# Kernel optimization log

Measured on AMD Instinct MI355X. Metric: run time of the kernel, lower is better.

The kernel has to match this reference:

```python
import jax, jax.numpy as jnp
import numpy as np

HIDDEN = 1024
NUM_HEADS = 16
HEAD_DIM = 64
B, S = 2, 2048


def setup_inputs() -> dict:
    key = jax.random.key(0)
    k1, k2, k3 = jax.random.split(key, 3)
    x = jax.random.normal(k1, (B, S, HIDDEN), dtype=jnp.float32)
    # xavier-uniform style scaling for the projection weights
    lim_qkv = (6.0 / (HIDDEN + 3 * NUM_HEADS * HEAD_DIM)) ** 0.5
    lim_o = (6.0 / (NUM_HEADS * HEAD_DIM + HIDDEN)) ** 0.5
    w_qkv = jax.random.uniform(k2, (HIDDEN, 3 * NUM_HEADS * HEAD_DIM), jnp.float32, -lim_qkv, lim_qkv)
    w_o = jax.random.uniform(k3, (NUM_HEADS * HEAD_DIM, HIDDEN), jnp.float32, -lim_o, lim_o)
    return {"x": x, "w_qkv": w_qkv, "w_o": w_o}


def reference(x, w_qkv, w_o):
    b, s, _ = x.shape
    qkv = jnp.einsum('bsh,hf->bsf', x, w_qkv)               # [b, s, 3*H*D]
    qkv = qkv.reshape(b, s, 3, NUM_HEADS, HEAD_DIM)
    q = jnp.transpose(qkv[:, :, 0], (0, 2, 1, 3))           # [b, h, s, d]
    k = jnp.transpose(qkv[:, :, 1], (0, 2, 3, 1))           # [b, h, d, s]
    v = jnp.transpose(qkv[:, :, 2], (0, 2, 1, 3))           # [b, h, s, d]
    scores = jnp.einsum('bhqd,bhdk->bhqk', q, k) / jnp.sqrt(jnp.float32(HEAD_DIM))
    scores = jax.nn.softmax(scores, axis=-1)                # [b, h, q, k]
    # NOTE: faithful to source bug: sums over q, output indexed by k
    values = jnp.einsum('bhqk,bhkd->bhkd', scores, v)       # [b, h, s, d]
    values = jnp.transpose(values, (0, 2, 1, 3)).reshape(b, s, NUM_HEADS * HEAD_DIM)
    return jnp.einsum('bsf,fh->bsh', values, w_o)
```

## Files before the change

### kernel.cpp

```cpp
#include <hip/hip_runtime.h>
#include <stdint.h>


#define DEV static __device__ __forceinline__

typedef unsigned short u16;
typedef __attribute__((ext_vector_type(4))) float f32x4;
typedef __attribute__((ext_vector_type(16))) float f32x16;
typedef __bf16 bf16x8 __attribute__((ext_vector_type(8)));
typedef __attribute__((ext_vector_type(8))) unsigned short u16x8;
typedef __attribute__((ext_vector_type(4))) unsigned short u16x4;

#define QSCALE 0.18033688011112042f

DEV u16 f2bf(float f) {
    unsigned u = __builtin_bit_cast(unsigned, f);
    u += 0x7fffu + ((u >> 16) & 1u);
    return (u16)(u >> 16);
}
DEV float bf2f(u16 h) {
    unsigned u = ((unsigned)h) << 16;
    return __builtin_bit_cast(float, u);
}

DEV void async_copy16(const void* g, void* l) {
    __builtin_amdgcn_global_load_lds(
        (__attribute__((address_space(1))) void*)(g),
        (__attribute__((address_space(3))) void*)(l), 16, 0, 0);
}


DEV void transpose_tile(const float* __restrict__ src, u16* __restrict__ dst,
                        int rows, int cols, int bx, int by, int t, float* tile) {
    int c0 = bx * 32, r0 = by * 32;
    int tx = t & 31, ty = t >> 5;
#pragma unroll
    for (int i = 0; i < 4; i++)
        tile[(ty + i * 8) * 33 + tx] = src[(size_t)(r0 + ty + i * 8) * cols + c0 + tx];
    __syncthreads();
#pragma unroll
    for (int i = 0; i < 4; i++)
        dst[(size_t)(c0 + ty + i * 8) * rows + r0 + tx] = f2bf(tile[tx * 33 + ty + i * 8]);
}

__global__ __launch_bounds__(256) void prep(
    const float* __restrict__ x, const float* __restrict__ wqkv,
    const float* __restrict__ wo, u16* __restrict__ xb,
    u16* __restrict__ wqkvT, u16* __restrict__ woT) {
    __shared__ float tile[32 * 33];
    const int gid = blockIdx.x;
    const int t = threadIdx.x;
    if (gid < 4096) {
        int i = gid * 256 + t;
        f32x4 v = *(const f32x4*)(x + (size_t)i * 4);
        u16x4 o;
#pragma unroll
        for (int j = 0; j < 4; j++) o[j] = f2bf(v[j]);
        *(u16x4*)(xb + (size_t)i * 4) = o;
    } else if (gid < 7168) {
        int lid = gid - 4096;
        transpose_tile(wqkv, wqkvT, 1024, 3072, lid % 96, lid / 96, t, tile);
    } else {
        int lid = gid - 7168;
        transpose_tile(wo, woT, 1024, 1024, lid & 31, lid >> 5, t, tile);
    }
}

__global__ __launch_bounds__(256) void gemm_qkv(
    const u16* __restrict__ A, const u16* __restrict__ Bt,
    u16* __restrict__ qb, u16* __restrict__ kb, u16* __restrict__ vb) {
    __shared__ __align__(16) u16 smem[128 * 136];
    u16* As = smem;
    u16* Bs = smem + 4096;
    const int t = threadIdx.x;
    const int wave = t >> 6;
    const int lane = t & 63;
    const int quad = lane >> 4;
    const int l16 = lane & 15;
    const int wr = wave >> 1;
    const int wc = wave & 1;
    const int m0 = blockIdx.y * 128;
    const int n0 = blockIdx.x * 128;
    const int swz = (l16 >> 1) & 3;

    f32x4 acc[4][4];
#pragma unroll
    for (int i = 0; i < 4; i++)
#pragma unroll
        for (int j = 0; j < 4; j++) acc[i][j] = {0.f, 0.f, 0.f, 0.f};

    for (int kt = 0; kt < 1024; kt += 32) {
#pragma unroll
        for (int i = 0; i < 2; i++) {
            int idx = i * 256 + t;
            int row = idx >> 2, kc = (idx & 3) ^ ((idx >> 3) & 3);
            async_copy16(A + (size_t)(m0 + row) * 1024 + kt + kc * 8, &As[idx * 8]);
            async_copy16(Bt + (size_t)(n0 + row) * 1024 + kt + kc * 8, &Bs[idx * 8]);
        }
        __syncthreads();
        bf16x8 af[4], bfr[4];
#pragma unroll
        for (int mt = 0; mt < 4; mt++)
            af[mt] = *(const bf16x8*)&As[(wr * 64 + mt * 16 + l16) * 32 + (quad ^ swz) * 8];
#pragma unroll
        for (int nt = 0; nt < 4; nt++)
            bfr[nt] = *(const bf16x8*)&Bs[(wc * 64 + nt * 16 + l16) * 32 + (quad ^ swz) * 8];
#pragma unroll
        for (int mt = 0; mt < 4; mt++)
#pragma unroll
            for (int nt = 0; nt < 4; nt++)
                acc[mt][nt] = __builtin_amdgcn_mfma_f32_16x16x32_bf16(
                    af[mt], bfr[nt], acc[mt][nt], 0, 0, 0);
        __syncthreads();
    }

    const int tsel = n0 >> 10;
    u16* dst = tsel == 0 ? qb : (tsel == 1 ? kb : vb);
    const float scl = tsel == 0 ? QSCALE : 1.0f;
#pragma unroll
    for (int mt = 0; mt < 4; mt++)
#pragma unroll
        for (int nt = 0; nt < 4; nt++) {
            int nn = wc * 64 + nt * 16 + l16;
#pragma unroll
            for (int r = 0; r < 4; r++) {
                int mm = wr * 64 + mt * 16 + quad * 4 + r;
                smem[mm * 136 + nn] = f2bf(acc[mt][nt][r] * scl);
            }
        }
    __syncthreads();
    const int col0 = (l16) * 8;
    const int rowb = (t >> 4);
    const int h0 = (n0 & 1023) >> 6;
#pragma unroll
    for (int i = 0; i < 8; i++) {
        int row = i * 16 + rowb;
        u16x8 v = *(const u16x8*)&smem[row * 136 + col0];
        int h = h0 + (col0 >> 6), d = col0 & 63;
        int mm = m0 + row;
        int b = mm >> 11, s = mm & 2047;
        *(u16x8*)&dst[((size_t)((b * 16 + h) * 2048 + s)) * 64 + d] = v;
    }
}

__global__ __launch_bounds__(256) void attn_pass1(
    const u16* __restrict__ qb, const u16* __restrict__ kb,
    float* __restrict__ lp) {
    __shared__ __align__(16) u16 Ks0[256 * 32];
    __shared__ __align__(16) u16 Ks1[256 * 32];
    const int t = threadIdx.x;
    const int wave = t >> 6;
    const int lane = t & 63;
    const int l32 = lane & 31, half = lane >> 5;
    const int kchunk = blockIdx.x & 1;
    const int qblk = (blockIdx.x >> 1) & 15;
    const int bh = blockIdx.x >> 5;
    const int q0 = qblk * 128 + wave * 32;
    const int swz = (l32 >> 1) & 3;
    const int c0 = ((half ^ swz) & 3) * 8;
    const int c1 = (((2 + half) ^ swz) & 3) * 8;

    const u16* Qr = qb + (size_t)(bh * 2048 + q0 + l32) * 64 + half * 8;
    bf16x8 a[4];
#pragma unroll
    for (int f = 0; f < 4; f++) a[f] = *(const bf16x8*)&Qr[f * 16];

    const u16* Kbase = kb + (size_t)(bh * 2048 + kchunk * 1024) * 64;
    const int srow = t >> 2, sc = ((t & 3) ^ ((t >> 3) & 3)) * 8;

    float lsum[16];
#pragma unroll
    for (int r = 0; r < 16; r++) lsum[r] = 0.f;

    for (int kt = 0; kt < 4; kt++) {
#pragma unroll
        for (int rr = 0; rr < 4; rr++) {
            const u16* src = Kbase + (size_t)(kt * 256 + rr * 64 + srow) * 64 + sc;
            async_copy16(src, &Ks0[rr * 2048 + t * 8]);
            async_copy16(src + 32, &Ks1[rr * 2048 + t * 8]);
        }
        __syncthreads();
        f32x16 acc2[2];
#pragma unroll
        for (int sub = 0; sub < 8; sub++) {
            const int row = sub * 32 + l32;
            bf16x8 bfr[4];
            bfr[0] = *(const bf16x8*)&Ks0[row * 32 + c0];
            bfr[1] = *(const bf16x8*)&Ks0[row * 32 + c1];
            bfr[2] = *(const bf16x8*)&Ks1[row * 32 + c0];
            bfr[3] = *(const bf16x8*)&Ks1[row * 32 + c1];
            f32x16 acc;
#pragma unroll
            for (int r = 0; r < 16; r++) acc[r] = 0.f;
#pragma unroll
            for (int f = 0; f < 4; f++)
                acc = __builtin_amdgcn_mfma_f32_32x32x16_bf16(a[f], bfr[f], acc, 0, 0, 0);
            acc2[sub & 1] = acc;
            if (sub > 0) {
                f32x16 p = acc2[(sub - 1) & 1];
#pragma unroll
                for (int r = 0; r < 16; r++)
                    lsum[r] += __builtin_amdgcn_exp2f(p[r]);
            }
        }
        {
            f32x16 p = acc2[1];
#pragma unroll
            for (int r = 0; r < 16; r++)
                lsum[r] += __builtin_amdgcn_exp2f(p[r]);
        }
        __syncthreads();
    }
#pragma unroll
    for (int r = 0; r < 16; r++) {
        float v = lsum[r];
        v += __shfl_xor(v, 1);
        v += __shfl_xor(v, 2);
        v += __shfl_xor(v, 4);
        v += __shfl_xor(v, 8);
        v += __shfl_xor(v, 16);
        lsum[r] = v;
    }
    if (l32 == 0) {
        float* dst = lp + kchunk * 65536 + bh * 2048 + q0 + half * 4;
#pragma unroll
        for (int r = 0; r < 16; r++)
            dst[(r & 3) + 8 * (r >> 2)] = lsum[r];
    }
}

__global__ __launch_bounds__(256) void attn_pass2(
    const u16* __restrict__ qb, const u16* __restrict__ kb,
    const float* __restrict__ lp, float* __restrict__ cp) {
    __shared__ __align__(16) u16 Qs0[256 * 32];
    __shared__ __align__(16) u16 Qs1[256 * 32];
    __shared__ __align__(16) float li_lds[1024];
    const int t = threadIdx.x;
    const int wave = t >> 6;
    const int lane = t & 63;
    const int l32 = lane & 31, half = lane >> 5;
    const int qchunk = blockIdx.x & 1;
    const int kblk = (blockIdx.x >> 1) & 15;
    const int bh = blockIdx.x >> 5;
    const int k0 = kblk * 128 + wave * 32;
    const int swz = (l32 >> 1) & 3;
    const int c0 = ((half ^ swz) & 3) * 8;
    const int c1 = (((2 + half) ^ swz) & 3) * 8;

    {
        const int base = bh * 2048 + qchunk * 1024;
        f32x4 p0 = *(const f32x4*)&lp[base + t * 4];
        f32x4 p1 = *(const f32x4*)&lp[65536 + base + t * 4];
        f32x4 li;
#pragma unroll
        for (int j = 0; j < 4; j++) li[j] = 1.0f / (p0[j] + p1[j]);
        *(f32x4*)&li_lds[t * 4] = li;
    }

    const u16* Kr = kb + (size_t)(bh * 2048 + k0 + l32) * 64 + half * 8;
    bf16x8 b[4];
#pragma unroll
    for (int f = 0; f < 4; f++) b[f] = *(const bf16x8*)&Kr[f * 16];

    const u16* Qbase = qb + (size_t)(bh * 2048 + qchunk * 1024) * 64;
    const int srow = t >> 2, sc = ((t & 3) ^ ((t >> 3) & 3)) * 8;

    float cs = 0.f;
    __syncthreads();

    for (int qt = 0; qt < 4; qt++) {
#pragma unroll
        for (int rr = 0; rr < 4; rr++) {
            const u16* src = Qbase + (size_t)(qt * 256 + rr * 64 + srow) * 64 + sc;
            async_copy16(src, &Qs0[rr * 2048 + t * 8]);
            async_copy16(src + 32, &Qs1[rr * 2048 + t * 8]);
        }
        __syncthreads();
        f32x16 acc2[2];
#pragma unroll
        for (int sub = 0; sub < 8; sub++) {
            const int row = sub * 32 + l32;
            bf16x8 af[4];
            af[0] = *(const bf16x8*)&Qs0[row * 32 + c0];
            af[1] = *(const bf16x8*)&Qs0[row * 32 + c1];
            af[2] = *(const bf16x8*)&Qs1[row * 32 + c0];
            af[3] = *(const bf16x8*)&Qs1[row * 32 + c1];
            f32x16 acc;
#pragma unroll
            for (int r = 0; r < 16; r++) acc[r] = 0.f;
#pragma unroll
            for (int f = 0; f < 4; f++)
                acc = __builtin_amdgcn_mfma_f32_32x32x16_bf16(af[f], b[f], acc, 0, 0, 0);
            acc2[sub & 1] = acc;
            if (sub > 0) {
                f32x16 p = acc2[(sub - 1) & 1];
                const float* lr = &li_lds[qt * 256 + (sub - 1) * 32 + half * 4];
#pragma unroll
                for (int g = 0; g < 4; g++) {
                    f32x4 li = *(const f32x4*)&lr[g * 8];
#pragma unroll
                    for (int r = 0; r < 4; r++)
                        cs += __builtin_amdgcn_exp2f(p[g * 4 + r]) * li[r];
                }
            }
        }
        {
            f32x16 p = acc2[1];
            const float* lr = &li_lds[qt * 256 + 7 * 32 + half * 4];
#pragma unroll
            for (int g = 0; g < 4; g++) {
                f32x4 li = *(const f32x4*)&lr[g * 8];
#pragma unroll
                for (int r = 0; r < 4; r++)
                    cs += __builtin_amdgcn_exp2f(p[g * 4 + r]) * li[r];
            }
        }
        __syncthreads();
    }
    cs += __shfl_xor(cs, 32);
    if (lane < 32)
        cp[qchunk * 65536 + bh * 2048 + k0 + lane] = cs;
}

__global__ __launch_bounds__(256) void gemm_out(
    const u16* __restrict__ vb, const float* __restrict__ cp,
    const u16* __restrict__ Bt, float* __restrict__ out) {
    __shared__ __align__(16) u16 As[64 * 32];
    __shared__ __align__(16) u16 Bs[128 * 32];
    const int m0 = blockIdx.y * 64;
    const int n0 = blockIdx.x * 128;
    const int t = threadIdx.x;
    const int wave = t >> 6, lane = t & 63;
    const int quad = lane >> 4, l16 = lane & 15;
    const int wr = wave >> 1, wc = wave & 1;
    const int swz = (l16 >> 1) & 3;

    const int mm = m0 + (t >> 2);
    const int b = mm >> 11, s = mm & 2047;
    const int cswz = (t & 3) ^ ((t >> 3) & 3);

    f32x4 acc[2][4];
#pragma unroll
    for (int i = 0; i < 2; i++)
#pragma unroll
        for (int j = 0; j < 4; j++) acc[i][j] = {0.f, 0.f, 0.f, 0.f};

    for (int kt = 0; kt < 1024; kt += 32) {
        {
            int k0 = kt + cswz * 8;
            int h = k0 >> 6, d = k0 & 63;
            int ci = (b * 16 + h) * 2048 + s;
            float csc = cp[ci] + cp[65536 + ci];
            u16x8 v = *(const u16x8*)&vb[((size_t)ci) * 64 + d];
            u16x8 o;
#pragma unroll
            for (int j = 0; j < 8; j++) o[j] = f2bf(bf2f(v[j]) * csc);
            *(u16x8*)&As[t * 8] = o;
        }
#pragma unroll
        for (int i = 0; i < 2; i++) {
            int idx = i * 256 + t;
            int row = idx >> 2, kc = (idx & 3) ^ ((idx >> 3) & 3);
            async_copy16(Bt + (size_t)(n0 + row) * 1024 + kt + kc * 8, &Bs[idx * 8]);
        }
        __syncthreads();
        bf16x8 af[2], bfr[4];
#pragma unroll
        for (int mt = 0; mt < 2; mt++)
            af[mt] = *(const bf16x8*)&As[(wr * 32 + mt * 16 + l16) * 32 + (quad ^ swz) * 8];
#pragma unroll
        for (int nt = 0; nt < 4; nt++)
            bfr[nt] = *(const bf16x8*)&Bs[(wc * 64 + nt * 16 + l16) * 32 + (quad ^ swz) * 8];
#pragma unroll
        for (int mt = 0; mt < 2; mt++)
#pragma unroll
            for (int nt = 0; nt < 4; nt++)
                acc[mt][nt] = __builtin_amdgcn_mfma_f32_16x16x32_bf16(
                    af[mt], bfr[nt], acc[mt][nt], 0, 0, 0);
        __syncthreads();
    }
#pragma unroll
    for (int nt = 0; nt < 4; nt++) {
        int nn = n0 + wc * 64 + nt * 16 + l16;
#pragma unroll
        for (int mt = 0; mt < 2; mt++) {
#pragma unroll
            for (int r = 0; r < 4; r++) {
                int mr = m0 + wr * 32 + mt * 16 + quad * 4 + r;
                out[(size_t)mr * 1024 + nn] = acc[mt][nt][r];
            }
        }
    }
}


extern "C" void kernel_launch(void* const* d_in, const int* in_sizes, int n_in,
                              void* d_out, int out_size, void* d_ws, size_t ws_size,
                              hipStream_t stream) {
    const float* x    = (const float*)d_in[0];
    const float* wqkv = (const float*)d_in[1];
    const float* wo   = (const float*)d_in[2];
    float* out = (float*)d_out;
    char* ws = (char*)d_ws;

    u16* xb      = (u16*)(ws);
    u16* wqkvT   = (u16*)(ws + 8388608);
    u16* woT     = (u16*)(ws + 14680064);
    u16* qb      = (u16*)(ws + 16777216);
    u16* kb      = (u16*)(ws + 25165824);
    u16* vb      = (u16*)(ws + 33554432);
    float* lp    = (float*)(ws);
    float* cp    = (float*)(ws + 1048576);

    prep<<<8192, 256, 0, stream>>>(x, wqkv, wo, xb, wqkvT, woT);
    gemm_qkv<<<dim3(24, 32), 256, 0, stream>>>(xb, wqkvT, qb, kb, vb);
    attn_pass1<<<1024, 256, 0, stream>>>(qb, kb, lp);
    attn_pass2<<<1024, 256, 0, stream>>>(qb, kb, lp, cp);
    gemm_out<<<dim3(8, 64), 256, 0, stream>>>(vb, cp, woT, out);
}
```

Before: 209.1 us.

## Split attention passes into four sequence chunks with smaller LDS tiles

```diff
diff --git a/kernel.cpp b/kernel.cpp
--- a/kernel.cpp
+++ b/kernel.cpp
@@ -143,18 +143,18 @@
     }
 }
 
-__global__ __launch_bounds__(256) void attn_pass1(
+__global__ __launch_bounds__(256, 8) void attn_pass1(
     const u16* __restrict__ qb, const u16* __restrict__ kb,
     float* __restrict__ lp) {
-    __shared__ __align__(16) u16 Ks0[256 * 32];
-    __shared__ __align__(16) u16 Ks1[256 * 32];
+    __shared__ __align__(16) u16 Ks0[128 * 32];
+    __shared__ __align__(16) u16 Ks1[128 * 32];
     const int t = threadIdx.x;
     const int wave = t >> 6;
     const int lane = t & 63;
     const int l32 = lane & 31, half = lane >> 5;
-    const int kchunk = blockIdx.x & 1;
-    const int qblk = (blockIdx.x >> 1) & 15;
-    const int bh = blockIdx.x >> 5;
+    const int kchunk = blockIdx.x & 3;
+    const int qblk = (blockIdx.x >> 2) & 15;
+    const int bh = blockIdx.x >> 6;
     const int q0 = qblk * 128 + wave * 32;
     const int swz = (l32 >> 1) & 3;
     const int c0 = ((half ^ swz) & 3) * 8;
@@ -165,7 +165,7 @@
 #pragma unroll
     for (int f = 0; f < 4; f++) a[f] = *(const bf16x8*)&Qr[f * 16];
 
-    const u16* Kbase = kb + (size_t)(bh * 2048 + kchunk * 1024) * 64;
+    const u16* Kbase = kb + (size_t)(bh * 2048 + kchunk * 512) * 64;
     const int srow = t >> 2, sc = ((t & 3) ^ ((t >> 3) & 3)) * 8;
 
     float lsum[16];
@@ -174,40 +174,33 @@
 
     for (int kt = 0; kt < 4; kt++) {
 #pragma unroll
-        for (int rr = 0; rr < 4; rr++) {
-            const u16* src = Kbase + (size_t)(kt * 256 + rr * 64 + srow) * 64 + sc;
+        for (int rr = 0; rr < 2; rr++) {
+            const u16* src = Kbase + (size_t)(kt * 128 + rr * 64 + srow) * 64 + sc;
             async_copy16(src, &Ks0[rr * 2048 + t * 8]);
             async_copy16(src + 32, &Ks1[rr * 2048 + t * 8]);
         }
         __syncthreads();
-        f32x16 acc2[2];
-#pragma unroll
-        for (int sub = 0; sub < 8; sub++) {
+#pragma unroll
+        for (int sub = 0; sub < 4; sub++) {
             const int row = sub * 32 + l32;
-            bf16x8 bfr[4];
-            bfr[0] = *(const bf16x8*)&Ks0[row * 32 + c0];
-            bfr[1] = *(const bf16x8*)&Ks0[row * 32 + c1];
-            bfr[2] = *(const bf16x8*)&Ks1[row * 32 + c0];
-            bfr[3] = *(const bf16x8*)&Ks1[row * 32 + c1];
             f32x16 acc;
 #pragma unroll
             for (int r = 0; r < 16; r++) acc[r] = 0.f;
-#pragma unroll
-            for (int f = 0; f < 4; f++)
-                acc = __builtin_amdgcn_mfma_f32_32x32x16_bf16(a[f], bfr[f], acc, 0, 0, 0);
-            acc2[sub & 1] = acc;
-            if (sub > 0) {
-                f32x16 p = acc2[(sub - 1) & 1];
-#pragma unroll
-                for (int r = 0; r < 16; r++)
-                    lsum[r] += __builtin_amdgcn_exp2f(p[r]);
-            }
-        }
-        {
-            f32x16 p = acc2[1];
+            {
+                bf16x8 b0 = *(const bf16x8*)&Ks0[row * 32 + c0];
+                bf16x8 b1 = *(const bf16x8*)&Ks0[row * 32 + c1];
+                acc = __builtin_amdgcn_mfma_f32_32x32x16_bf16(a[0], b0, acc, 0, 0, 0);
+                acc = __builtin_amdgcn_mfma_f32_32x32x16_bf16(a[1], b1, acc, 0, 0, 0);
+            }
+            {
+                bf16x8 b2 = *(const bf16x8*)&Ks1[row * 32 + c0];
+                bf16x8 b3 = *(const bf16x8*)&Ks1[row * 32 + c1];
+                acc = __builtin_amdgcn_mfma_f32_32x32x16_bf16(a[2], b2, acc, 0, 0, 0);
+                acc = __builtin_amdgcn_mfma_f32_32x32x16_bf16(a[3], b3, acc, 0, 0, 0);
+            }
 #pragma unroll
             for (int r = 0; r < 16; r++)
-                lsum[r] += __builtin_amdgcn_exp2f(p[r]);
+                lsum[r] += __builtin_amdgcn_exp2f(acc[r]);
         }
         __syncthreads();
     }
@@ -229,32 +222,33 @@
     }
 }
 
-__global__ __launch_bounds__(256) void attn_pass2(
+__global__ __launch_bounds__(256, 8) void attn_pass2(
     const u16* __restrict__ qb, const u16* __restrict__ kb,
     const float* __restrict__ lp, float* __restrict__ cp) {
-    __shared__ __align__(16) u16 Qs0[256 * 32];
-    __shared__ __align__(16) u16 Qs1[256 * 32];
-    __shared__ __align__(16) float li_lds[1024];
+    __shared__ __align__(16) u16 Qs0[128 * 32];
+    __shared__ __align__(16) u16 Qs1[128 * 32];
+    __shared__ __align__(16) float li_lds[512];
     const int t = threadIdx.x;
     const int wave = t >> 6;
     const int lane = t & 63;
     const int l32 = lane & 31, half = lane >> 5;
-    const int qchunk = blockIdx.x & 1;
-    const int kblk = (blockIdx.x >> 1) & 15;
-    const int bh = blockIdx.x >> 5;
+    const int qchunk = blockIdx.x & 3;
+    const int kblk = (blockIdx.x >> 2) & 15;
+    const int bh = blockIdx.x >> 6;
     const int k0 = kblk * 128 + wave * 32;
     const int swz = (l32 >> 1) & 3;
     const int c0 = ((half ^ swz) & 3) * 8;
     const int c1 = (((2 + half) ^ swz) & 3) * 8;
 
     {
-        const int base = bh * 2048 + qchunk * 1024;
-        f32x4 p0 = *(const f32x4*)&lp[base + t * 4];
-        f32x4 p1 = *(const f32x4*)&lp[65536 + base + t * 4];
-        f32x4 li;
-#pragma unroll
-        for (int j = 0; j < 4; j++) li[j] = 1.0f / (p0[j] + p1[j]);
-        *(f32x4*)&li_lds[t * 4] = li;
+        const int base = bh * 2048 + qchunk * 512;
+#pragma unroll
+        for (int j = 0; j < 2; j++) {
+            int i = t + j * 256;
+            float p = lp[base + i] + lp[65536 + base + i] +
+                      lp[131072 + base + i] + lp[196608 + base + i];
+            li_lds[i] = 1.0f / p;
+        }
     }
 
     const u16* Kr = kb + (size_t)(bh * 2048 + k0 + l32) * 64 + half * 8;
@@ -262,7 +256,7 @@
 #pragma unroll
     for (int f = 0; f < 4; f++) b[f] = *(const bf16x8*)&Kr[f * 16];
 
-    const u16* Qbase = qb + (size_t)(bh * 2048 + qchunk * 1024) * 64;
+    const u16* Qbase = qb + (size_t)(bh * 2048 + qchunk * 512) * 64;
     const int srow = t >> 2, sc = ((t & 3) ^ ((t >> 3) & 3)) * 8;
 
     float cs = 0.f;
@@ -270,49 +264,37 @@
 
     for (int qt = 0; qt < 4; qt++) {
 #pragma unroll
-        for (int rr = 0; rr < 4; rr++) {
-            const u16* src = Qbase + (size_t)(qt * 256 + rr * 64 + srow) * 64 + sc;
+        for (int rr = 0; rr < 2; rr++) {
+            const u16* src = Qbase + (size_t)(qt * 128 + rr * 64 + srow) * 64 + sc;
             async_copy16(src, &Qs0[rr * 2048 + t * 8]);
             async_copy16(src + 32, &Qs1[rr * 2048 + t * 8]);
         }
         __syncthreads();
-        f32x16 acc2[2];
-#pragma unroll
-        for (int sub = 0; sub < 8; sub++) {
+#pragma unroll
+        for (int sub = 0; sub < 4; sub++) {
             const int row = sub * 32 + l32;
-            bf16x8 af[4];
-            af[0] = *(const bf16x8*)&Qs0[row * 32 + c0];
-            af[1] = *(const bf16x8*)&Qs0[row * 32 + c1];
-            af[2] = *(const bf16x8*)&Qs1[row * 32 + c0];
-            af[3] = *(const bf16x8*)&Qs1[row * 32 + c1];
             f32x16 acc;
 #pragma unroll
             for (int r = 0; r < 16; r++) acc[r] = 0.f;
-#pragma unroll
-            for (int f = 0; f < 4; f++)
-                acc = __builtin_amdgcn_mfma_f32_32x32x16_bf16(af[f], b[f], acc, 0, 0, 0);
-            acc2[sub & 1] = acc;
-            if (sub > 0) {
-                f32x16 p = acc2[(sub - 1) & 1];
-                const float* lr = &li_lds[qt * 256 + (sub - 1) * 32 + half * 4];
-#pragma unroll
-                for (int g = 0; g < 4; g++) {
-                    f32x4 li = *(const f32x4*)&lr[g * 8];
-#pragma unroll
-                    for (int r = 0; r < 4; r++)
-                        cs += __builtin_amdgcn_exp2f(p[g * 4 + r]) * li[r];
-                }
-            }
-        }
-        {
-            f32x16 p = acc2[1];
-            const float* lr = &li_lds[qt * 256 + 7 * 32 + half * 4];
+            {
+                bf16x8 a0 = *(const bf16x8*)&Qs0[row * 32 + c0];
+                bf16x8 a1 = *(const bf16x8*)&Qs0[row * 32 + c1];
+                acc = __builtin_amdgcn_mfma_f32_32x32x16_bf16(a0, b[0], acc, 0, 0, 0);
+                acc = __builtin_amdgcn_mfma_f32_32x32x16_bf16(a1, b[1], acc, 0, 0, 0);
+            }
+            {
+                bf16x8 a2 = *(const bf16x8*)&Qs1[row * 32 + c0];
+                bf16x8 a3 = *(const bf16x8*)&Qs1[row * 32 + c1];
+                acc = __builtin_amdgcn_mfma_f32_32x32x16_bf16(a2, b[2], acc, 0, 0, 0);
+                acc = __builtin_amdgcn_mfma_f32_32x32x16_bf16(a3, b[3], acc, 0, 0, 0);
+            }
+            const float* lr = &li_lds[qt * 128 + sub * 32 + half * 4];
 #pragma unroll
             for (int g = 0; g < 4; g++) {
                 f32x4 li = *(const f32x4*)&lr[g * 8];
 #pragma unroll
                 for (int r = 0; r < 4; r++)
-                    cs += __builtin_amdgcn_exp2f(p[g * 4 + r]) * li[r];
+                    cs += __builtin_amdgcn_exp2f(acc[g * 4 + r]) * li[r];
             }
         }
         __syncthreads();
@@ -350,7 +332,7 @@
             int k0 = kt + cswz * 8;
             int h = k0 >> 6, d = k0 & 63;
             int ci = (b * 16 + h) * 2048 + s;
-            float csc = cp[ci] + cp[65536 + ci];
+            float csc = cp[ci] + cp[65536 + ci] + cp[131072 + ci] + cp[196608 + ci];
             u16x8 v = *(const u16x8*)&vb[((size_t)ci) * 64 + d];
             u16x8 o;
 #pragma unroll
@@ -414,7 +396,7 @@
 
     prep<<<8192, 256, 0, stream>>>(x, wqkv, wo, xb, wqkvT, woT);
     gemm_qkv<<<dim3(24, 32), 256, 0, stream>>>(xb, wqkvT, qb, kb, vb);
-    attn_pass1<<<1024, 256, 0, stream>>>(qb, kb, lp);
-    attn_pass2<<<1024, 256, 0, stream>>>(qb, kb, lp, cp);
+    attn_pass1<<<2048, 256, 0, stream>>>(qb, kb, lp);
+    attn_pass2<<<2048, 256, 0, stream>>>(qb, kb, lp, cp);
     gemm_out<<<dim3(8, 64), 256, 0, stream>>>(vb, cp, woT, out);
 }
```

After: 377.3 us. 80.5% more time.
